# Performance work log

Measured on AMD Instinct MI355X. Metric: run time of the kernel, lower is better.

The kernel has to match this reference:

```python
import jax, jax.numpy as jnp
import numpy as np

B, S, D, K = 4, 8192, 512, 20


def setup_inputs() -> dict:
    key = jax.random.key(0)
    k1, k2, k3, k4 = jax.random.split(key, 4)
    std = 0.02  # _init_weights: normal(0, 0.02/sqrt(layer_idx+1)), layer_idx=0
    return {
        "x": jax.random.normal(k1, (B, S, D), dtype=jnp.float32),
        "positions": jax.random.normal(k2, (K, D), dtype=jnp.float32) * 0.2,
        "log_scales": jnp.log(1.0 + 0.5 * jax.random.uniform(k3, (K,), dtype=jnp.float32)),
        "amplitudes": 1.2 + 0.3 * jax.random.uniform(k4, (K,), dtype=jnp.float32),
        "w_v": jax.random.normal(jax.random.fold_in(key, 10), (D, D), dtype=jnp.float32) * std,
        "w_o": jax.random.normal(jax.random.fold_in(key, 11), (D, D), dtype=jnp.float32) * std,
    }


def reference(x, positions, log_scales, amplitudes, w_v, w_o):
    # Gaussian-splat RBF attention (token -> splat -> token routing).
    scales = jnp.exp(log_scales)  # [K]
    # squared distances ||x - c||^2 via expansion (avoids [B,S,K,D] tensor)
    x2 = jnp.sum(x * x, axis=-1, keepdims=True)           # [B,S,1]
    c2 = jnp.sum(positions * positions, axis=-1)          # [K]
    xc = jnp.einsum('bsd,kd->bsk', x, positions)          # [B,S,K]
    d2 = jnp.maximum(x2 - 2.0 * xc + c2, 0.0)             # [B,S,K]
    gauss = amplitudes * jnp.exp(-0.5 * d2 / (scales * scales))  # [B,S,K]
    attn = gauss / (jnp.sum(gauss, axis=-1, keepdims=True) + 1e-8)  # per-token normalize
    v = jnp.einsum('bsd,ed->bse', x, w_v)                 # token_value_proj (no bias)
    splat_states = jnp.einsum('bsk,bsd->bkd', attn, v)    # gather token values at splats
    out = jnp.einsum('bsk,bkd->bsd', attn, splat_states)  # scatter back to tokens
    return jnp.einsum('bsd,ed->bse', out, w_o)            # output_proj (dropout=eval identity)
```

## Files before the change

### kernel.cpp

```cpp
#include <hip/hip_runtime.h>
#include <hip/hip_bf16.h>

#define BB 4
#define SS 8192
#define DD 512
#define KK 20
#define GG 8
#define BKD (BB * KK * DD)

__device__ __forceinline__ float dot4(float4 a, float4 b) {
  return a.x * b.x + a.y * b.y + a.z * b.z + a.w * b.w;
}

__global__ void k0_params(const float* __restrict__ pos,
                          const float* __restrict__ log_scales,
                          const float* __restrict__ amps,
                          float* __restrict__ params) {
  int k = blockIdx.x;
  int lane = threadIdx.x;
  float acc = 0.f;
  for (int d = lane; d < DD; d += 64) { float p = pos[k * DD + d]; acc += p * p; }
#pragma unroll
  for (int off = 32; off > 0; off >>= 1) acc += __shfl_xor(acc, off);
  if (lane == 0) {
    params[k] = acc;
    float s = __expf(log_scales[k]);
    params[KK + k] = 0.5f / (s * s);
    params[2 * KK + k] = amps[k];
  }
}

__global__ __launch_bounds__(256) void kA_attn(
    const float* __restrict__ x, const float* __restrict__ pos,
    const float* __restrict__ params, float* __restrict__ attn_g) {
  __shared__ float pos_s[KK * DD];
  __shared__ float prm_s[3 * KK];
  int tid = threadIdx.x;
  for (int i = tid; i < KK * DD / 4; i += 256)
    ((float4*)pos_s)[i] = ((const float4*)pos)[i];
  if (tid < 3 * KK) prm_s[tid] = params[tid];
  __syncthreads();

  int b = blockIdx.x >> 7;
  int c = blockIdx.x & 127;
  size_t row0 = (size_t)b * SS + (size_t)c * 64;
  int q = tid >> 4;
  int dsub = tid & 15;

  const float* xq = x + (row0 + q) * DD;

  float acc[4][KK];
  float x2[4];
#pragma unroll
  for (int r = 0; r < 4; ++r) {
    x2[r] = 0.f;
#pragma unroll
    for (int k = 0; k < KK; ++k) acc[r][k] = 0.f;
  }

#pragma unroll 2
  for (int j = 0; j < 8; ++j) {
    int d0 = j * 64 + dsub * 4;
    float4 xv[4];
#pragma unroll
    for (int r = 0; r < 4; ++r) xv[r] = *(const float4*)(xq + (size_t)(r * 16) * DD + d0);
#pragma unroll
    for (int r = 0; r < 4; ++r) x2[r] += dot4(xv[r], xv[r]);
#pragma unroll
    for (int k = 0; k < KK; ++k) {
      float4 p = *(const float4*)(pos_s + k * DD + d0);
#pragma unroll
      for (int r = 0; r < 4; ++r) acc[r][k] += dot4(xv[r], p);
    }
  }

#pragma unroll
  for (int r = 0; r < 4; ++r) {
#pragma unroll
    for (int m = 1; m <= 8; m <<= 1) x2[r] += __shfl_xor(x2[r], m);
#pragma unroll
    for (int k = 0; k < KK; ++k) {
#pragma unroll
      for (int m = 1; m <= 8; m <<= 1) acc[r][k] += __shfl_xor(acc[r][k], m);
    }
  }

  if (dsub == 0) {
#pragma unroll
    for (int r = 0; r < 4; ++r) {
      float gg[KK];
      float sum = 0.f;
#pragma unroll
      for (int k = 0; k < KK; ++k) {
        float d2 = fmaxf(x2[r] - 2.f * acc[r][k] + prm_s[k], 0.f);
        gg[k] = prm_s[2 * KK + k] * __expf(-prm_s[KK + k] * d2);
        sum += gg[k];
      }
      float inv = 1.f / (sum + 1e-8f);
      float* ar = attn_g + (row0 + q + r * 16) * KK;
#pragma unroll
      for (int k = 0; k < KK; ++k) ar[k] = gg[k] * inv;
    }
  }
}

__global__ __launch_bounds__(256) void kB_scatter(
    const float* __restrict__ x, const float* __restrict__ attn,
    float* __restrict__ Mpart, int tpc) {
  int t = threadIdx.x;
  int c = blockIdx.x;
  int b = blockIdx.y;
  int cpb = gridDim.x;
  size_t row0 = (size_t)b * SS + (size_t)c * tpc;

  float2 Ml[KK];
#pragma unroll
  for (int k = 0; k < KK; ++k) Ml[k] = make_float2(0.f, 0.f);

  const float* xb = x + row0 * DD + 2 * t;
  const float* ab = attn + row0 * KK;
  for (int s = 0; s < tpc; ++s) {
    float2 xv = *(const float2*)(xb + (size_t)s * DD);
    const float4* ar4 = (const float4*)(ab + s * KK);
#pragma unroll
    for (int kk = 0; kk < KK / 4; ++kk) {
      float4 a4 = ar4[kk];
      Ml[4 * kk + 0].x += a4.x * xv.x; Ml[4 * kk + 0].y += a4.x * xv.y;
      Ml[4 * kk + 1].x += a4.y * xv.x; Ml[4 * kk + 1].y += a4.y * xv.y;
      Ml[4 * kk + 2].x += a4.z * xv.x; Ml[4 * kk + 2].y += a4.z * xv.y;
      Ml[4 * kk + 3].x += a4.w * xv.x; Ml[4 * kk + 3].y += a4.w * xv.y;
    }
  }
  float* mp = Mpart + ((size_t)b * cpb + c) * KK * DD + 2 * t;
#pragma unroll
  for (int k = 0; k < KK; ++k) *(float2*)(mp + (size_t)k * DD) = Ml[k];
}

__global__ __launch_bounds__(256) void kC1_reduce(
    const float* __restrict__ Mpart, float* __restrict__ red8,
    int cpb, int cpg) {
  int idx = blockIdx.x * 256 + threadIdx.x;
  int g = idx / BKD;
  int rem = idx - g * BKD;
  int b = rem / (KK * DD);
  int kd = rem - b * (KK * DD);
  const float* p = Mpart + ((size_t)b * cpb + (size_t)g * cpg) * KK * DD + kd;
  float acc = 0.f;
#pragma unroll 8
  for (int c = 0; c < cpg; ++c) acc += p[(size_t)c * KK * DD];
  red8[idx] = acc;
}

__global__ __launch_bounds__(512) void k3f8(
    const float* __restrict__ red8, const float* __restrict__ w_v,
    const float* __restrict__ w_o, float* __restrict__ ws2) {
  __shared__ float m_s[DD];
  __shared__ float v_s[DD];
  int bk = blockIdx.x;
  int e = threadIdx.x;

  const float* p = red8 + (size_t)bk * DD + e;
  float acc = 0.f;
#pragma unroll
  for (int g = 0; g < GG; ++g) acc += p[(size_t)g * BKD];
  m_s[e] = acc;
  __syncthreads();

  const float4* wr = (const float4*)(w_v + (size_t)e * DD);
  float a2 = 0.f;
#pragma unroll 4
  for (int j = 0; j < DD / 4; ++j) a2 += dot4(((const float4*)m_s)[j], wr[j]);
  v_s[e] = a2;
  __syncthreads();

  const float4* wr2 = (const float4*)(w_o + (size_t)e * DD);
  float a3 = 0.f;
#pragma unroll 4
  for (int j = 0; j < DD / 4; ++j) a3 += dot4(((const float4*)v_s)[j], wr2[j]);
  ws2[(size_t)bk * DD + e] = a3;
}

__global__ __launch_bounds__(256) void k5_gather(
    const float* __restrict__ attn, const float* __restrict__ ws2,
    float* __restrict__ out) {
  int tid = threadIdx.x;
  int b = blockIdx.x >> 9;
  int sc = blockIdx.x & 511;
  size_t s0 = (size_t)sc * 16;
  int tr = tid >> 7;
  int e4 = tid & 127;

  float4 w[KK];
  const float* wb = ws2 + (size_t)b * KK * DD + e4 * 4;
#pragma unroll
  for (int k = 0; k < KK; ++k) w[k] = *(const float4*)(wb + (size_t)k * DD);

  size_t rowA = (size_t)b * SS + s0 + tr;
  const float* ar = attn + rowA * KK;
  float* orow = out + rowA * DD + e4 * 4;

#pragma unroll 2
  for (int i = 0; i < 8; ++i) {
    const float4* a4 = (const float4*)(ar + (size_t)2 * i * KK);
    float4 A = a4[0], Bv = a4[1], C = a4[2], Dv = a4[3], E = a4[4];
    float4 o = make_float4(0.f, 0.f, 0.f, 0.f);
#define ACC(av, kbase) \
    o.x += av * w[kbase].x; o.y += av * w[kbase].y; \
    o.z += av * w[kbase].z; o.w += av * w[kbase].w;
    ACC(A.x, 0)  ACC(A.y, 1)  ACC(A.z, 2)  ACC(A.w, 3)
    ACC(Bv.x, 4) ACC(Bv.y, 5) ACC(Bv.z, 6) ACC(Bv.w, 7)
    ACC(C.x, 8)  ACC(C.y, 9)  ACC(C.z, 10) ACC(C.w, 11)
    ACC(Dv.x, 12) ACC(Dv.y, 13) ACC(Dv.z, 14) ACC(Dv.w, 15)
    ACC(E.x, 16) ACC(E.y, 17) ACC(E.z, 18) ACC(E.w, 19)
#undef ACC
    *(float4*)(orow + (size_t)2 * i * DD) = o;
  }
}

extern "C" void kernel_launch(void* const* d_in, const int* in_sizes, int n_in,
                              void* d_out, int out_size, void* d_ws, size_t ws_size,
                              hipStream_t stream) {
  const float* x   = (const float*)d_in[0];
  const float* pos = (const float*)d_in[1];
  const float* ls  = (const float*)d_in[2];
  const float* am  = (const float*)d_in[3];
  const float* w_v = (const float*)d_in[4];
  const float* w_o = (const float*)d_in[5];
  float* out = (float*)d_out;

  float* ws     = (float*)d_ws;
  float* attn   = ws;
  float* ws2    = attn + (size_t)BB * SS * KK;
  float* params = ws2 + (size_t)BB * KK * DD;
  float* red8   = params + 64;
  float* Mpart  = red8 + (size_t)GG * BKD;

  size_t head_f = (size_t)BB * SS * KK + (size_t)BB * KK * DD + 64 + (size_t)GG * BKD;
  int cpb = 256, tpc = 32;
  size_t need = (head_f + (size_t)BB * cpb * KK * DD) * sizeof(float);
  if (ws_size < need) { cpb = 128; tpc = 64; }
  int cpg = cpb / GG;

  k0_params<<<KK, 64, 0, stream>>>(pos, ls, am, params);
  kA_attn<<<512, 256, 0, stream>>>(x, pos, params, attn);
  kB_scatter<<<dim3(cpb, BB), 256, 0, stream>>>(x, attn, Mpart, tpc);
  kC1_reduce<<<(GG * BKD) / 256, 256, 0, stream>>>(Mpart, red8, cpb, cpg);
  k3f8<<<BB * KK, 512, 0, stream>>>(red8, w_v, w_o, ws2);
  k5_gather<<<2048, 256, 0, stream>>>(attn, ws2, out);
}
```

Baseline: 290.9 us.

## Split fused double GEMV into two wave-per-row GEMV launches and halve scatter chunks

The single 80-block kernel that applied w_v then w_o with one thread per output row is replaced by two launches of a GEMV kernel spread over 640 blocks. Each wave computes a dot product per row using coalesced float4 loads and a shuffle reduction, and a new buffer holds the intermediate between the two launches. The aim is better parallelism and coalesced weight reads in place of strided per-thread row reads. The scatter chunk count is also cut from 256 to 128 per batch, which shrinks the partial buffers and the reduce traffic but gives each scatter block more serial work.

```diff
diff --git a/kernel.cpp b/kernel.cpp
--- a/kernel.cpp
+++ b/kernel.cpp
@@ -151,33 +151,42 @@
   red8[idx] = acc;
 }
 
-__global__ __launch_bounds__(512) void k3f8(
-    const float* __restrict__ red8, const float* __restrict__ w_v,
-    const float* __restrict__ w_o, float* __restrict__ ws2) {
+__global__ __launch_bounds__(256) void kP_gemv(
+    const float* __restrict__ in, const float* __restrict__ W,
+    float* __restrict__ out, int mode) {
   __shared__ float m_s[DD];
-  __shared__ float v_s[DD];
+  int tid = threadIdx.x;
   int bk = blockIdx.x;
-  int e = threadIdx.x;
-
-  const float* p = red8 + (size_t)bk * DD + e;
-  float acc = 0.f;
-#pragma unroll
-  for (int g = 0; g < GG; ++g) acc += p[(size_t)g * BKD];
-  m_s[e] = acc;
+  int et = blockIdx.y;
+
+  for (int i = tid; i < DD; i += 256) {
+    float a;
+    if (mode == 0) {
+      const float* p = in + (size_t)bk * DD + i;
+      a = 0.f;
+#pragma unroll
+      for (int g = 0; g < GG; ++g) a += p[(size_t)g * BKD];
+    } else {
+      a = in[(size_t)bk * DD + i];
+    }
+    m_s[i] = a;
+  }
   __syncthreads();
 
-  const float4* wr = (const float4*)(w_v + (size_t)e * DD);
-  float a2 = 0.f;
+  int wave = tid >> 6;
+  int lane = tid & 63;
+  float4 ma = ((const float4*)m_s)[lane];
+  float4 mb = ((const float4*)m_s)[64 + lane];
+
 #pragma unroll 4
-  for (int j = 0; j < DD / 4; ++j) a2 += dot4(((const float4*)m_s)[j], wr[j]);
-  v_s[e] = a2;
-  __syncthreads();
-
-  const float4* wr2 = (const float4*)(w_o + (size_t)e * DD);
-  float a3 = 0.f;
-#pragma unroll 4
-  for (int j = 0; j < DD / 4; ++j) a3 += dot4(((const float4*)v_s)[j], wr2[j]);
-  ws2[(size_t)bk * DD + e] = a3;
+  for (int rr = 0; rr < 16; ++rr) {
+    int e = et * 64 + wave * 16 + rr;
+    const float4* wrow = (const float4*)(W + (size_t)e * DD);
+    float p = dot4(wrow[lane], ma) + dot4(wrow[64 + lane], mb);
+#pragma unroll
+    for (int m = 1; m <= 32; m <<= 1) p += __shfl_xor(p, m);
+    if (lane == 0) out[(size_t)bk * DD + e] = p;
+  }
 }
 
 __global__ __launch_bounds__(256) void k5_gather(
@@ -231,20 +240,22 @@
   float* ws     = (float*)d_ws;
   float* attn   = ws;
   float* ws2    = attn + (size_t)BB * SS * KK;
-  float* params = ws2 + (size_t)BB * KK * DD;
+  float* ssb    = ws2 + (size_t)BB * KK * DD;
+  float* params = ssb + (size_t)BB * KK * DD;
   float* red8   = params + 64;
   float* Mpart  = red8 + (size_t)GG * BKD;
 
-  size_t head_f = (size_t)BB * SS * KK + (size_t)BB * KK * DD + 64 + (size_t)GG * BKD;
-  int cpb = 256, tpc = 32;
+  size_t head_f = (size_t)BB * SS * KK + 2 * (size_t)BB * KK * DD + 64 + (size_t)GG * BKD;
+  int cpb = 128, tpc = 64;
   size_t need = (head_f + (size_t)BB * cpb * KK * DD) * sizeof(float);
-  if (ws_size < need) { cpb = 128; tpc = 64; }
+  if (ws_size < need) { cpb = 64; tpc = 128; }
   int cpg = cpb / GG;
 
   k0_params<<<KK, 64, 0, stream>>>(pos, ls, am, params);
   kA_attn<<<512, 256, 0, stream>>>(x, pos, params, attn);
   kB_scatter<<<dim3(cpb, BB), 256, 0, stream>>>(x, attn, Mpart, tpc);
   kC1_reduce<<<(GG * BKD) / 256, 256, 0, stream>>>(Mpart, red8, cpb, cpg);
-  k3f8<<<BB * KK, 512, 0, stream>>>(red8, w_v, w_o, ws2);
+  kP_gemv<<<dim3(BB * KK, 8), 256, 0, stream>>>(red8, w_v, ssb, 0);
+  kP_gemv<<<dim3(BB * KK, 8), 256, 0, stream>>>(ssb, w_o, ws2, 1);
   k5_gather<<<2048, 256, 0, stream>>>(attn, ws2, out);
 }
```

Result: faster. 256.9 us (-11.7%).
